# Optimization experiments

Measured on AMD Instinct MI355X. Metric: run time of the kernel, lower is better.

The kernel has to match this reference:

```python
import jax, jax.numpy as jnp
import numpy as np

GROUP_SIZE = 128


def setup_inputs() -> dict:
    key = jax.random.key(0)
    kx, kw = jax.random.split(key)
    x = jax.random.normal(kx, (4, 2048, 4096), dtype=jnp.float32)
    weight = jax.random.normal(kw, (11008, 4096), dtype=jnp.float32) * 0.02
    return {"x": x, "weight": weight}


def reference(x, weight):
    # Training-path forward of OneBitLinear (bias=False, group_size=128):
    # per-128-group L-inf scale, STE-sign binarization, rescale, then dense linear.
    O, I = weight.shape                      # [out, in]
    G = GROUP_SIZE
    wg = weight.reshape(O, I // G, G)        # [out, num_groups, group]
    scales = jnp.clip(jnp.max(jnp.abs(wg), axis=-1, keepdims=True), 1e-8)
    w_sign = jnp.sign(wg / scales)           # {-1, 0, +1}
    w_eff = (w_sign * scales).reshape(O, I)  # effective 1-bit weight in fp32
    # F.linear: x @ w_eff.T  -> [batch, seq, out]
    return jnp.einsum('bsi,oi->bso', x, w_eff)
```

## Files before the change

kernel.cpp:

```cpp
#include <hip/hip_runtime.h>

#define M_DIM 8192
#define K_DIM 4096
#define N_DIM 11008
#define BM 256
#define BN 256
#define BK 64
#define TILES_M (M_DIM / BM)
#define TILES_N (N_DIM / BN)
#define NT (K_DIM / BK)
#define NWG (TILES_M * TILES_N)

typedef __attribute__((ext_vector_type(8))) short bf16x8;
typedef __attribute__((ext_vector_type(4))) float f32x4;
typedef __attribute__((ext_vector_type(8))) unsigned short u16x8;

__device__ __forceinline__ unsigned short f2bf_rne(float f) {
    unsigned int u = __float_as_uint(f);
    unsigned int r = (u + 0x7FFFu + ((u >> 16) & 1u)) >> 16;
    return (unsigned short)r;
}

__device__ __forceinline__ void gload_lds16(const void* g, void* l) {
    __builtin_amdgcn_global_load_lds(
        (const __attribute__((address_space(1))) void*)g,
        (__attribute__((address_space(3))) void*)l, 16, 0, 0);
}

__global__ __launch_bounds__(256) void cast_x_kernel(const float* __restrict__ x,
                                                     unsigned short* __restrict__ xb) {
    size_t t = (size_t)blockIdx.x * 256 + threadIdx.x;
    const float4* p = reinterpret_cast<const float4*>(x) + 2 * t;
    float4 a = p[0];
    float4 b = p[1];
    u16x8 o;
    o[0] = f2bf_rne(a.x); o[1] = f2bf_rne(a.y); o[2] = f2bf_rne(a.z); o[3] = f2bf_rne(a.w);
    o[4] = f2bf_rne(b.x); o[5] = f2bf_rne(b.y); o[6] = f2bf_rne(b.z); o[7] = f2bf_rne(b.w);
    *reinterpret_cast<u16x8*>(xb + 8 * t) = o;
}

__global__ __launch_bounds__(256) void binarize_w_kernel(const float* __restrict__ w,
                                                         unsigned short* __restrict__ weff) {
    size_t t = (size_t)blockIdx.x * 256 + threadIdx.x;
    size_t group = t >> 5;
    int l32 = (int)(t & 31);
    const float4* src = reinterpret_cast<const float4*>(w + group * 128) + l32;
    float4 v = *src;
    float amax = fmaxf(fmaxf(fabsf(v.x), fabsf(v.y)), fmaxf(fabsf(v.z), fabsf(v.w)));
#pragma unroll
    for (int off = 16; off >= 1; off >>= 1)
        amax = fmaxf(amax, __shfl_xor(amax, off));
    float scale = fmaxf(amax, 1e-8f);
    unsigned short pb = f2bf_rne(scale);
    unsigned short nb = (unsigned short)(pb | 0x8000u);
    ushort4 o;
    o.x = (v.x == 0.0f) ? (unsigned short)0 : ((v.x > 0.0f) ? pb : nb);
    o.y = (v.y == 0.0f) ? (unsigned short)0 : ((v.y > 0.0f) ? pb : nb);
    o.z = (v.z == 0.0f) ? (unsigned short)0 : ((v.z > 0.0f) ? pb : nb);
    o.w = (v.w == 0.0f) ? (unsigned short)0 : ((v.w > 0.0f) ? pb : nb);
    *reinterpret_cast<ushort4*>(weff + group * 128 + (size_t)l32 * 4) = o;
}

__global__ __launch_bounds__(512, 2) void gemm_bin_kernel(
        const unsigned short* __restrict__ A,
        const unsigned short* __restrict__ B,
        float* __restrict__ C) {
    __shared__ unsigned short lds[2][2][2][8192];

    const int bid = blockIdx.x;
    const int swz = (bid & 7) * (NWG / 8) + (bid >> 3);
    const int tm = swz / TILES_N;
    const int tn = swz % TILES_N;

    const int tid = threadIdx.x;
    const int wave = tid >> 6;
    const int lane = tid & 63;
    const int wm = wave >> 2;
    const int wn = wave & 3;
    const int l15 = lane & 15;
    const int l4  = lane >> 4;

    const int srow  = tid >> 3;
    const int gslot = (tid & 7) ^ (srow & 7);
    const unsigned short* Asrc = A + (size_t)(tm * BM + srow) * K_DIM + gslot * 8;
    const unsigned short* Bsrc = B + (size_t)(tn * BN + srow) * K_DIM + gslot * 8;

    auto stageA = [&](int buf, int half, int kt) {
        const unsigned short* s = Asrc + (size_t)(half * 128) * K_DIM + kt;
        unsigned short* d = &lds[buf][0][half][tid * 8];
        gload_lds16(s, d);
        gload_lds16(s + (size_t)64 * K_DIM, d + 4096);
    };
    auto stageB = [&](int buf, int half, int kt) {
        const unsigned short* s = Bsrc + (size_t)(half * 128) * K_DIM + kt;
        unsigned short* d = &lds[buf][1][half][tid * 8];
        gload_lds16(s, d);
        gload_lds16(s + (size_t)64 * K_DIM, d + 4096);
    };
    auto readfrag = [&](const unsigned short* base, int rowl, int ks) -> bf16x8 {
        return *reinterpret_cast<const bf16x8*>(
            &base[rowl * 64 + (((ks * 4 + l4) ^ (rowl & 7)) * 8)]);
    };

    f32x4 acc[8][4] = {};
    bf16x8 bf[4][2];

    stageA(0, 0, 0); stageA(0, 1, 0);
    stageB(0, 0, 0); stageB(0, 1, 0);
    stageB(1, 0, BK); stageB(1, 1, BK);
    asm volatile("s_waitcnt vmcnt(4)" ::: "memory");
    __builtin_amdgcn_s_barrier();

    for (int t = 0; t < NT; ++t) {
        const int c = t & 1;
        const unsigned short* Ah = &lds[c][0][wm][0];
        const unsigned short* Bh = &lds[c][1][wn >> 1][0];
        const int brow0 = (wn & 1) * 64;

#pragma unroll
        for (int q = 0; q < 4; ++q) {
            bf16x8 af[2][2];
            if (q == 0) {
#pragma unroll
                for (int j = 0; j < 4; ++j)
#pragma unroll
                    for (int ks = 0; ks < 2; ++ks)
                        bf[j][ks] = readfrag(Bh, brow0 + j * 16 + l15, ks);
            }
#pragma unroll
            for (int r = 0; r < 2; ++r)
#pragma unroll
                for (int ks = 0; ks < 2; ++ks)
                    af[r][ks] = readfrag(Ah, (2 * q + r) * 16 + l15, ks);

            if (q == 0 && t + 1 < NT) stageA(c ^ 1, 0, (t + 1) * BK);
            if (q == 1 && t + 1 < NT) stageA(c ^ 1, 1, (t + 1) * BK);
            if (q == 2 && t + 2 < NT) stageB(c, 0, (t + 2) * BK);
            if (q == 3 && t + 2 < NT) stageB(c, 1, (t + 2) * BK);

            __builtin_amdgcn_s_barrier();
            asm volatile("s_waitcnt lgkmcnt(0)" ::: "memory");
            __builtin_amdgcn_s_setprio(1);
#pragma unroll
            for (int ks = 0; ks < 2; ++ks)
#pragma unroll
                for (int r = 0; r < 2; ++r)
#pragma unroll
                    for (int j = 0; j < 4; ++j)
                        acc[2 * q + r][j] = __builtin_amdgcn_mfma_f32_16x16x32_bf16(
                            af[r][ks], bf[j][ks], acc[2 * q + r][j], 0, 0, 0);
            __builtin_amdgcn_s_setprio(0);
            if (q == 3) {
                if (t < NT - 2) asm volatile("s_waitcnt vmcnt(4)" ::: "memory");
                else            asm volatile("s_waitcnt vmcnt(0)" ::: "memory");
            }
            __builtin_amdgcn_s_barrier();
        }
    }

    const size_t crow0 = (size_t)tm * BM + wm * 128 + l4 * 4;
    const int ccol0 = tn * BN + wn * 64 + l15;
#pragma unroll
    for (int i = 0; i < 8; ++i) {
#pragma unroll
        for (int j = 0; j < 4; ++j) {
            float* cp = C + (crow0 + i * 16) * N_DIM + ccol0 + j * 16;
#pragma unroll
            for (int r = 0; r < 4; ++r)
                cp[(size_t)r * N_DIM] = acc[i][j][r];
        }
    }
}

extern "C" void kernel_launch(void* const* d_in, const int* in_sizes, int n_in,
                              void* d_out, int out_size, void* d_ws, size_t ws_size,
                              hipStream_t stream) {
    const float* x = (const float*)d_in[0];
    const float* w = (const float*)d_in[1];
    float* out = (float*)d_out;

    unsigned short* xb = (unsigned short*)d_ws;
    unsigned short* weff = (unsigned short*)((char*)d_ws + (size_t)M_DIM * K_DIM * 2);

    cast_x_kernel<<<(M_DIM * K_DIM / 8) / 256, 256, 0, stream>>>(x, xb);
    binarize_w_kernel<<<(N_DIM * K_DIM / 4) / 256, 256, 0, stream>>>(w, weff);
    gemm_bin_kernel<<<NWG, 512, 0, stream>>>(xb, weff, out);
}
```

Measured before the change: 733.5 us.

## Software-pipeline LDS fragment reads with MFMA using double-buffered register fragments

Restructures the GEMM main loop so LDS fragment reads for the next quarter (and next k-tile's B fragments) are issued between MFMA batches, with ping-pong register buffers and a manually 2x unrolled k loop. This removes the lgkmcnt(0) stall before each MFMA group and lets LDS latency hide behind matrix math, and the vmcnt wait is tightened and moved. It also switches output stores to nontemporal. Register pressure rises with extra fragment buffers, risking spills under the 512x2 launch bound, and barrier placement changes could introduce races.

After: 742.9 us. Within noise of the previous version (+1.3%).

```diff
diff --git a/kernel.cpp b/kernel.cpp
--- a/kernel.cpp
+++ b/kernel.cpp
@@ -79,6 +79,7 @@
     const int wn = wave & 3;
     const int l15 = lane & 15;
     const int l4  = lane >> 4;
+    const int brow0 = (wn & 1) * 64;
 
     const int srow  = tid >> 3;
     const int gslot = (tid & 7) ^ (srow & 7);
@@ -103,59 +104,87 @@
     };
 
     f32x4 acc[8][4] = {};
-    bf16x8 bf[4][2];
+    bf16x8 bfA[4][2], bfB[4][2], af0[2][2], af1[2][2];
+
+#define READ_A(DST, BASE, Q)                                                    \
+    {                                                                           \
+        _Pragma("unroll") for (int r_ = 0; r_ < 2; ++r_) {                      \
+            _Pragma("unroll") for (int ks_ = 0; ks_ < 2; ++ks_) {               \
+                DST[r_][ks_] = readfrag(BASE, (2 * (Q) + r_) * 16 + l15, ks_);  \
+            }                                                                   \
+        }                                                                       \
+    }
+#define READ_B(DST, BASE)                                                       \
+    {                                                                           \
+        _Pragma("unroll") for (int j_ = 0; j_ < 4; ++j_) {                      \
+            _Pragma("unroll") for (int ks_ = 0; ks_ < 2; ++ks_) {               \
+                DST[j_][ks_] = readfrag(BASE, brow0 + j_ * 16 + l15, ks_);      \
+            }                                                                   \
+        }                                                                       \
+    }
+#define MFMA8(AF, BF, Q, KS)                                                    \
+    {                                                                           \
+        _Pragma("unroll") for (int r_ = 0; r_ < 2; ++r_) {                      \
+            _Pragma("unroll") for (int j_ = 0; j_ < 4; ++j_) {                  \
+                acc[2 * (Q) + r_][j_] = __builtin_amdgcn_mfma_f32_16x16x32_bf16(\
+                    AF[r_][KS], BF[j_][KS], acc[2 * (Q) + r_][j_], 0, 0, 0);    \
+            }                                                                   \
+        }                                                                       \
+    }
 
     stageA(0, 0, 0); stageA(0, 1, 0);
     stageB(0, 0, 0); stageB(0, 1, 0);
     stageB(1, 0, BK); stageB(1, 1, BK);
     asm volatile("s_waitcnt vmcnt(4)" ::: "memory");
     __builtin_amdgcn_s_barrier();
-
-    for (int t = 0; t < NT; ++t) {
-        const int c = t & 1;
-        const unsigned short* Ah = &lds[c][0][wm][0];
-        const unsigned short* Bh = &lds[c][1][wn >> 1][0];
-        const int brow0 = (wn & 1) * 64;
-
-#pragma unroll
-        for (int q = 0; q < 4; ++q) {
-            bf16x8 af[2][2];
-            if (q == 0) {
-#pragma unroll
-                for (int j = 0; j < 4; ++j)
-#pragma unroll
-                    for (int ks = 0; ks < 2; ++ks)
-                        bf[j][ks] = readfrag(Bh, brow0 + j * 16 + l15, ks);
-            }
-#pragma unroll
-            for (int r = 0; r < 2; ++r)
-#pragma unroll
-                for (int ks = 0; ks < 2; ++ks)
-                    af[r][ks] = readfrag(Ah, (2 * q + r) * 16 + l15, ks);
-
-            if (q == 0 && t + 1 < NT) stageA(c ^ 1, 0, (t + 1) * BK);
-            if (q == 1 && t + 1 < NT) stageA(c ^ 1, 1, (t + 1) * BK);
-            if (q == 2 && t + 2 < NT) stageB(c, 0, (t + 2) * BK);
-            if (q == 3 && t + 2 < NT) stageB(c, 1, (t + 2) * BK);
-
-            __builtin_amdgcn_s_barrier();
-            asm volatile("s_waitcnt lgkmcnt(0)" ::: "memory");
-            __builtin_amdgcn_s_setprio(1);
-#pragma unroll
-            for (int ks = 0; ks < 2; ++ks)
-#pragma unroll
-                for (int r = 0; r < 2; ++r)
-#pragma unroll
-                    for (int j = 0; j < 4; ++j)
-                        acc[2 * q + r][j] = __builtin_amdgcn_mfma_f32_16x16x32_bf16(
-                            af[r][ks], bf[j][ks], acc[2 * q + r][j], 0, 0, 0);
-            __builtin_amdgcn_s_setprio(0);
-            if (q == 3) {
-                if (t < NT - 2) asm volatile("s_waitcnt vmcnt(4)" ::: "memory");
-                else            asm volatile("s_waitcnt vmcnt(0)" ::: "memory");
-            }
-            __builtin_amdgcn_s_barrier();
-        }
+    READ_B(bfA, (&lds[0][1][wn >> 1][0]));
+    READ_A(af0, (&lds[0][0][wm][0]), 0);
+
+#define KTILE(T, CUR, NXT, BF, BFN)                                             \
+    {                                                                           \
+        const unsigned short* Ah  = &lds[CUR][0][wm][0];                        \
+        const unsigned short* Ahn = &lds[NXT][0][wm][0];                        \
+        const unsigned short* Bhn = &lds[NXT][1][wn >> 1][0];                   \
+                                                                        \
+        if ((T) + 1 < NT) stageA(NXT, 0, ((T) + 1) * BK);                       \
+        __builtin_amdgcn_s_setprio(1);                                          \
+        MFMA8(af0, BF, 0, 0);                                                   \
+        READ_A(af1, Ah, 1);                                                     \
+        MFMA8(af0, BF, 0, 1);                                                   \
+        __builtin_amdgcn_s_setprio(0);                                          \
+        __builtin_amdgcn_s_barrier();                                           \
+                                                                        \
+        if ((T) + 1 < NT) stageA(NXT, 1, ((T) + 1) * BK);                       \
+        __builtin_amdgcn_s_setprio(1);                                          \
+        MFMA8(af1, BF, 1, 0);                                                   \
+        READ_A(af0, Ah, 2);                                                     \
+        MFMA8(af1, BF, 1, 1);                                                   \
+        __builtin_amdgcn_s_setprio(0);                                          \
+        __builtin_amdgcn_s_barrier();                                           \
+                                                                        \
+        if ((T) + 2 < NT) stageB(CUR, 0, ((T) + 2) * BK);                       \
+        __builtin_amdgcn_s_setprio(1);                                          \
+        MFMA8(af0, BF, 2, 0);                                                   \
+        READ_A(af1, Ah, 3);                                                     \
+        MFMA8(af0, BF, 2, 1);                                                   \
+        __builtin_amdgcn_s_setprio(0);                                          \
+        if ((T) + 2 < NT) { asm volatile("s_waitcnt vmcnt(2)" ::: "memory"); }  \
+        else              { asm volatile("s_waitcnt vmcnt(0)" ::: "memory"); }  \
+        __builtin_amdgcn_s_barrier();                                           \
+                        \
+        if ((T) + 2 < NT) stageB(CUR, 1, ((T) + 2) * BK);                       \
+        __builtin_amdgcn_s_setprio(1);                                          \
+        MFMA8(af1, BF, 3, 0);                                                   \
+        if ((T) + 1 < NT) { READ_B(BFN, Bhn); READ_A(af0, Ahn, 0); }            \
+        MFMA8(af1, BF, 3, 1);                                                   \
+        __builtin_amdgcn_s_setprio(0);                                          \
+        __builtin_amdgcn_s_barrier();                                           \
+    }
+
+#pragma unroll 1
+    for (int tt = 0; tt < NT; tt += 2) {
+        KTILE(tt,     0, 1, bfA, bfB);
+        KTILE(tt + 1, 1, 0, bfB, bfA);
     }
 
     const size_t crow0 = (size_t)tm * BM + wm * 128 + l4 * 4;
@@ -167,7 +196,7 @@
             float* cp = C + (crow0 + i * 16) * N_DIM + ccol0 + j * 16;
 #pragma unroll
             for (int r = 0; r < 4; ++r)
-                cp[(size_t)r * N_DIM] = acc[i][j][r];
+                __builtin_nontemporal_store(acc[i][j][r], cp + (size_t)r * N_DIM);
         }
     }
 }
```

## Shrink M tile to 128 and load B fragments directly into registers

Applied to the files above, without the earlier changes.

Halves the M tile and the workgroup size. Only A is staged through LDS; each wave loads its B fragments straight from global memory into double-buffered registers. The k-loop is restructured around a full wait and barrier per tile, and the output uses nontemporal stores. The aim is to cut LDS traffic and barrier count, at the cost of less reuse of B across the tile, more total global reads, and less latency hiding.

After: 1.892 ms. +157.9%, slower.

```diff
diff --git a/kernel.cpp b/kernel.cpp
--- a/kernel.cpp
+++ b/kernel.cpp
@@ -3,7 +3,7 @@
 #define M_DIM 8192
 #define K_DIM 4096
 #define N_DIM 11008
-#define BM 256
+#define BM 128
 #define BN 256
 #define BK 64
 #define TILES_M (M_DIM / BM)
@@ -61,11 +61,11 @@
     *reinterpret_cast<ushort4*>(weff + group * 128 + (size_t)l32 * 4) = o;
 }
 
-__global__ __launch_bounds__(512, 2) void gemm_bin_kernel(
+__global__ __launch_bounds__(256, 2) void gemm_bin_kernel(
         const unsigned short* __restrict__ A,
         const unsigned short* __restrict__ B,
         float* __restrict__ C) {
-    __shared__ unsigned short lds[2][2][2][8192];
+    __shared__ unsigned short As[2][BM * BK];
 
     const int bid = blockIdx.x;
     const int swz = (bid & 7) * (NWG / 8) + (bid >> 3);
@@ -75,91 +75,82 @@
     const int tid = threadIdx.x;
     const int wave = tid >> 6;
     const int lane = tid & 63;
-    const int wm = wave >> 2;
-    const int wn = wave & 3;
     const int l15 = lane & 15;
     const int l4  = lane >> 4;
 
     const int srow  = tid >> 3;
     const int gslot = (tid & 7) ^ (srow & 7);
     const unsigned short* Asrc = A + (size_t)(tm * BM + srow) * K_DIM + gslot * 8;
-    const unsigned short* Bsrc = B + (size_t)(tn * BN + srow) * K_DIM + gslot * 8;
 
-    auto stageA = [&](int buf, int half, int kt) {
-        const unsigned short* s = Asrc + (size_t)(half * 128) * K_DIM + kt;
-        unsigned short* d = &lds[buf][0][half][tid * 8];
-        gload_lds16(s, d);
-        gload_lds16(s + (size_t)64 * K_DIM, d + 4096);
+    auto stageA = [&](int buf, int kt) {
+#pragma unroll
+        for (int cc = 0; cc < 4; ++cc)
+            gload_lds16(Asrc + (size_t)(cc * 32) * K_DIM + kt,
+                        &As[buf][cc * 2048 + tid * 8]);
     };
-    auto stageB = [&](int buf, int half, int kt) {
-        const unsigned short* s = Bsrc + (size_t)(half * 128) * K_DIM + kt;
-        unsigned short* d = &lds[buf][1][half][tid * 8];
-        gload_lds16(s, d);
-        gload_lds16(s + (size_t)64 * K_DIM, d + 4096);
-    };
-    auto readfrag = [&](const unsigned short* base, int rowl, int ks) -> bf16x8 {
+    auto readA = [&](int buf, int i, int ks) -> bf16x8 {
+        int row = i * 16 + l15;
         return *reinterpret_cast<const bf16x8*>(
-            &base[rowl * 64 + (((ks * 4 + l4) ^ (rowl & 7)) * 8)]);
+            &As[buf][row * 64 + (((ks * 4 + l4) ^ (row & 7)) * 8)]);
     };
 
+    const unsigned short* Bp[4];
+#pragma unroll
+    for (int j = 0; j < 4; ++j)
+        Bp[j] = B + (size_t)(tn * BN + wave * 64 + j * 16 + l15) * K_DIM + l4 * 8;
+
     f32x4 acc[8][4] = {};
-    bf16x8 bf[4][2];
+    bf16x8 b0[4][2], b1[4][2], af0[4], af1[4];
 
-    stageA(0, 0, 0); stageA(0, 1, 0);
-    stageB(0, 0, 0); stageB(0, 1, 0);
-    stageB(1, 0, BK); stageB(1, 1, BK);
-    asm volatile("s_waitcnt vmcnt(4)" ::: "memory");
+#define LOAD_B(BANK, KT)                                                        \
+    { _Pragma("unroll") for (int j_ = 0; j_ < 4; ++j_) {                        \
+        BANK[j_][0] = *reinterpret_cast<const bf16x8*>(Bp[j_] + (KT));          \
+        BANK[j_][1] = *reinterpret_cast<const bf16x8*>(Bp[j_] + (KT) + 32); } }
+#define READ_A4(DST, BUF, H, KS)                                                \
+    { _Pragma("unroll") for (int r_ = 0; r_ < 4; ++r_)                          \
+        DST[r_] = readA(BUF, (H) * 4 + r_, KS); }
+#define MFMA16(AF, BANK, H, KS)                                                 \
+    { _Pragma("unroll") for (int r_ = 0; r_ < 4; ++r_) {                        \
+        _Pragma("unroll") for (int j_ = 0; j_ < 4; ++j_)                        \
+            acc[(H) * 4 + r_][j_] = __builtin_amdgcn_mfma_f32_16x16x32_bf16(    \
+                AF[r_], BANK[j_][KS], acc[(H) * 4 + r_][j_], 0, 0, 0); } }
+
+    stageA(0, 0);
+    LOAD_B(b0, 0);
+    asm volatile("s_waitcnt vmcnt(0)" ::: "memory");
     __builtin_amdgcn_s_barrier();
 
-    for (int t = 0; t < NT; ++t) {
-        const int c = t & 1;
-        const unsigned short* Ah = &lds[c][0][wm][0];
-        const unsigned short* Bh = &lds[c][1][wn >> 1][0];
-        const int brow0 = (wn & 1) * 64;
-
-#pragma unroll
-        for (int q = 0; q < 4; ++q) {
-            bf16x8 af[2][2];
-            if (q == 0) {
-#pragma unroll
-                for (int j = 0; j < 4; ++j)
-#pragma unroll
-                    for (int ks = 0; ks < 2; ++ks)
-                        bf[j][ks] = readfrag(Bh, brow0 + j * 16 + l15, ks);
-            }
-#pragma unroll
-            for (int r = 0; r < 2; ++r)
-#pragma unroll
-                for (int ks = 0; ks < 2; ++ks)
-                    af[r][ks] = readfrag(Ah, (2 * q + r) * 16 + l15, ks);
-
-            if (q == 0 && t + 1 < NT) stageA(c ^ 1, 0, (t + 1) * BK);
-            if (q == 1 && t + 1 < NT) stageA(c ^ 1, 1, (t + 1) * BK);
-            if (q == 2 && t + 2 < NT) stageB(c, 0, (t + 2) * BK);
-            if (q == 3 && t + 2 < NT) stageB(c, 1, (t + 2) * BK);
-
-            __builtin_amdgcn_s_barrier();
-            asm volatile("s_waitcnt lgkmcnt(0)" ::: "memory");
-            __builtin_amdgcn_s_setprio(1);
-#pragma unroll
-            for (int ks = 0; ks < 2; ++ks)
-#pragma unroll
-                for (int r = 0; r < 2; ++r)
-#pragma unroll
-                    for (int j = 0; j < 4; ++j)
-                        acc[2 * q + r][j] = __builtin_amdgcn_mfma_f32_16x16x32_bf16(
-                            af[r][ks], bf[j][ks], acc[2 * q + r][j], 0, 0, 0);
-            __builtin_amdgcn_s_setprio(0);
-            if (q == 3) {
-                if (t < NT - 2) asm volatile("s_waitcnt vmcnt(4)" ::: "memory");
-                else            asm volatile("s_waitcnt vmcnt(0)" ::: "memory");
-            }
-            __builtin_amdgcn_s_barrier();
-        }
+#define KTILE(T, CUR, NXT, BC, BN_)                                             \
+    {                                                                           \
+        if ((T) + 1 < NT) {                                                     \
+            stageA(NXT, ((T) + 1) * BK);                                        \
+            LOAD_B(BN_, ((T) + 1) * BK);                                        \
+            __builtin_amdgcn_sched_barrier(0);                                  \
+        }                                                                       \
+        READ_A4(af0, CUR, 0, 0);                                                \
+        __builtin_amdgcn_s_setprio(1);                                          \
+        READ_A4(af1, CUR, 1, 0);                                                \
+        MFMA16(af0, BC, 0, 0);                                                  \
+        READ_A4(af0, CUR, 0, 1);                                                \
+        MFMA16(af1, BC, 1, 0);                                                  \
+        READ_A4(af1, CUR, 1, 1);                                                \
+        MFMA16(af0, BC, 0, 1);                                                  \
+        MFMA16(af1, BC, 1, 1);                                                  \
+        __builtin_amdgcn_s_setprio(0);                                          \
+        if ((T) + 1 < NT) {                                                     \
+            asm volatile("s_waitcnt vmcnt(0)" ::: "memory");                    \
+            __builtin_amdgcn_s_barrier();                                       \
+        }                                                                       \
     }
 
-    const size_t crow0 = (size_t)tm * BM + wm * 128 + l4 * 4;
-    const int ccol0 = tn * BN + wn * 64 + l15;
+#pragma unroll 1
+    for (int tt = 0; tt < NT; tt += 2) {
+        KTILE(tt,     0, 1, b0, b1);
+        KTILE(tt + 1, 1, 0, b1, b0);
+    }
+
+    const size_t crow0 = (size_t)tm * BM + l4 * 4;
+    const int ccol0 = tn * BN + wave * 64 + l15;
 #pragma unroll
     for (int i = 0; i < 8; ++i) {
 #pragma unroll
@@ -167,7 +158,7 @@
             float* cp = C + (crow0 + i * 16) * N_DIM + ccol0 + j * 16;
 #pragma unroll
             for (int r = 0; r < 4; ++r)
-                cp[(size_t)r * N_DIM] = acc[i][j][r];
+                __builtin_nontemporal_store(acc[i][j][r], cp + (size_t)r * N_DIM);
         }
     }
 }
@@ -184,5 +175,5 @@
 
     cast_x_kernel<<<(M_DIM * K_DIM / 8) / 256, 256, 0, stream>>>(x, xb);
     binarize_w_kernel<<<(N_DIM * K_DIM / 4) / 256, 256, 0, stream>>>(w, weff);
-    gemm_bin_kernel<<<NWG, 512, 0, stream>>>(xb, weff, out);
+    gemm_bin_kernel<<<NWG, 256, 0, stream>>>(xb, weff, out);
 }
```
